# Optimization experiments

Measured on AMD Instinct MI355X. Metric: run time of the kernel, lower is better.

The kernel has to match this reference:

```python
import jax, jax.numpy as jnp
import numpy as np

B, T, K = 32, 512, 48
START_TAG, STOP_TAG = 46, 47


def setup_inputs() -> dict:
    key = jax.random.key(0)
    k1, k2, k3 = jax.random.split(key, 3)
    features = jax.random.normal(k1, (B, T, K, K), dtype=jnp.float32)
    targets = jax.random.randint(k2, (B, T), 0, K * K)  # flattened (from,to) index
    # lengths in [1, T], sorted descending (pack_padded_sequence convention)
    lengths = jnp.sort(jax.random.randint(k3, (B,), 1, T + 1))[::-1]
    return {"features": features, "targets": targets, "lengths": lengths}


def reference(features, targets, lengths):
    b, t_max, k, _ = features.shape
    # gold score: gather flattened target index per (b, t), masked by length
    flat = features.reshape(b, t_max, k * k)
    scores_at_targets = jnp.take_along_axis(flat, targets[:, :, None], axis=2)[:, :, 0]
    valid = jnp.arange(t_max)[None, :] < lengths[:, None]  # [B, T]
    gold_score = jnp.sum(jnp.where(valid, scores_at_targets, jnp.zeros((), features.dtype)))

    # forward (log-partition) recurrence; t=0 initializes from START row (all lengths >= 1)
    init = features[:, 0, START_TAG, :]  # [B, K]

    def step(carry, inp):
        feat_t, t = inp  # feat_t: [B, K, K] (prev_tag, cur_tag)
        cand = jax.nn.logsumexp(feat_t + carry[:, :, None], axis=1)  # [B, K]
        carry = jnp.where((t < lengths)[:, None], cand, carry)
        return carry, None

    feats_rest = jnp.moveaxis(features[:, 1:], 1, 0)  # [T-1, B, K, K]
    ts = jnp.arange(1, t_max)
    final, _ = jax.lax.scan(step, init, (feats_rest, ts))

    all_paths_scores = jnp.sum(final[:, STOP_TAG])
    return (all_paths_scores - gold_score) / b
```

## Files before the change

### kernel.cpp

```cpp
#include <hip/hip_runtime.h>

#define BB 32
#define TT 512
#define KK 48
#define KK2 2304
#define START_TAG 46
#define STOP_TAG 47
#define L2E 1.4426950408889634f
#define LN2 0.6931471805599453f
#define SLAB 7

__device__ inline float fast_exp2(float x) {
#if __has_builtin(__builtin_amdgcn_exp2f)
  return __builtin_amdgcn_exp2f(x);
#else
  return exp2f(x);
#endif
}
__device__ inline float fast_log2(float x) {
#if __has_builtin(__builtin_amdgcn_logf)
  return __builtin_amdgcn_logf(x);
#else
  return log2f(x);
#endif
}

template <int CTRL>
__device__ inline float dppf(float v) {
  int i = __float_as_int(v);
  int r = __builtin_amdgcn_update_dpp(i, i, CTRL, 0xF, 0xF, false);
  return __int_as_float(r);
}

__global__ __launch_bounds__(192, 1) void crf_kernel(
    const float* __restrict__ feat,
    const int* __restrict__ targets,
    const int* __restrict__ lengths,
    float* __restrict__ ws,
    float* __restrict__ out) {

  __shared__ float fbuf[2][SLAB * KK2];
  __shared__ float carry_g[2][KK];
  __shared__ float red[4];

  const int b   = blockIdx.x;
  const int len = lengths[b];
  const int tid = threadIdx.x;
  const int w   = tid >> 6;
  const int l   = tid & 63;
  const int j0  = l >> 2;
  const int ig  = l & 3;
  const int j   = w * 16 + j0;
  const float* fb = feat + (size_t)b * TT * KK2;

  float gsum = 0.f;
  for (int t = tid; t < TT; t += 192)
    if (t < len) gsum += fb[(size_t)t * KK2 + targets[b * TT + t]];
  #pragma unroll
  for (int m = 1; m < 64; m <<= 1) gsum += __shfl_xor(gsum, m, 64);
  if (l == 0) red[w] = gsum;

  if (tid < KK)
    carry_g[0][(tid & 3) * 12 + (tid >> 2)] = fb[START_TAG * KK + tid] * L2E;

  const int nsteps = len - 1;
  const int nslab  = (nsteps + SLAB - 1) / SLAB;

  auto stage_slab = [&](int s, int buf) {
    #pragma unroll
    for (int u = 0; u < SLAB; ++u) {
      int t = s * SLAB + 1 + u;
      if (t > len - 1) t = len - 1;
      #pragma unroll
      for (int q = 0; q < 3; ++q) {
        const float* gq = fb + (size_t)t * KK2 + (q * 16 + j0) * KK + w * 16 + ig * 4;
        float* d = &fbuf[buf][u * KK2 + w * 768 + q * 256];
        __builtin_amdgcn_global_load_lds(
            (const __attribute__((address_space(1))) unsigned int*)(const void*)gq,
            (__attribute__((address_space(3))) unsigned int*)(void*)d,
            16, 0, 0);
      }
    }
  };

  if (nsteps > 0) stage_slab(0, 0);
  __syncthreads();
  const float gold_b = red[0] + red[1] + red[2];

  for (int s = 0; s < nslab; ++s) {
    const int buf = s & 1;
    if (s + 1 < nslab) stage_slab(s + 1, buf ^ 1);
    const int base = s * SLAB + 1;
    const float* fs = &fbuf[buf][w * 768];

    float x[2][12];
    #pragma unroll
    for (int r = 0; r < 12; ++r) x[0][r] = fs[(r * 4 + ig) * 16 + j0];

    #pragma unroll
    for (int u = 0; u < SLAB; ++u) {
      const int t = base + u;
      if (t < len) {
        const int rd = (t - 1) & 1, wr = t & 1;

        float c[12];
        #pragma unroll
        for (int q = 0; q < 3; ++q) {
          float4 cv = *reinterpret_cast<const float4*>(&carry_g[rd][ig * 12 + q * 4]);
          c[q * 4 + 0] = cv.x; c[q * 4 + 1] = cv.y;
          c[q * 4 + 2] = cv.z; c[q * 4 + 3] = cv.w;
        }

        float xv[12];
        #pragma unroll
        for (int r = 0; r < 12; ++r) xv[r] = fmaf(x[u & 1][r], L2E, c[r]);

        if (u + 1 < SLAB) {
          #pragma unroll
          for (int r = 0; r < 12; ++r)
            x[(u + 1) & 1][r] = fs[(u + 1) * KK2 + (r * 4 + ig) * 16 + j0];
        }

        float m0 = fmaxf(fmaxf(xv[0], xv[1]), fmaxf(xv[2], xv[3]));
        float m1 = fmaxf(fmaxf(xv[4], xv[5]), fmaxf(xv[6], xv[7]));
        float m2 = fmaxf(fmaxf(xv[8], xv[9]), fmaxf(xv[10], xv[11]));
        float m = fmaxf(fmaxf(m0, m1), m2);
        m = fmaxf(m, dppf<0xB1>(m));
        m = fmaxf(m, dppf<0x4E>(m));

        float s0 = 0.f, s1 = 0.f, s2 = 0.f, s3 = 0.f;
        #pragma unroll
        for (int r = 0; r < 12; r += 4) {
          s0 += fast_exp2(xv[r + 0] - m);
          s1 += fast_exp2(xv[r + 1] - m);
          s2 += fast_exp2(xv[r + 2] - m);
          s3 += fast_exp2(xv[r + 3] - m);
        }
        float sm = (s0 + s1) + (s2 + s3);
        sm += dppf<0xB1>(sm);
        sm += dppf<0x4E>(sm);
        float cn = m + fast_log2(sm);

        if (ig == 0) carry_g[wr][(j & 3) * 12 + (j >> 2)] = cn;

        if (u == SLAB - 1) {
          asm volatile("s_waitcnt vmcnt(0) lgkmcnt(0)" ::: "memory");
        } else {
          asm volatile("s_waitcnt lgkmcnt(0)" ::: "memory");
        }
        __builtin_amdgcn_s_barrier();
      }
    }
  }

  if (tid == 0) {
    const int rdf = (len - 1) & 1;
    float v = carry_g[rdf][47] * LN2 - gold_b;
    atomicAdd(&ws[0], v);
    __threadfence();
    int done = atomicAdd((int*)&ws[1], 1);
    if (done == BB - 1) out[0] = atomicAdd(&ws[0], 0.0f) / (float)BB;
  }
}

extern "C" void kernel_launch(void* const* d_in, const int* in_sizes, int n_in,
                              void* d_out, int out_size, void* d_ws, size_t ws_size,
                              hipStream_t stream) {
  const float* feat  = (const float*)d_in[0];
  const int* targets = (const int*)d_in[1];
  const int* lengths = (const int*)d_in[2];
  float* ws  = (float*)d_ws;
  float* out = (float*)d_out;

  hipMemsetAsync(d_ws, 0, 16, stream);
  crf_kernel<<<BB, 192, 0, stream>>>(feat, targets, lengths, ws, out);
}
```

Before: 395.1 us.

## Stream features into registers via buffer loads and use lagged logsumexp shift

Replaces the LDS slab staging with raw buffer_load_dword instructions that land feature values directly in registers. Four per-step register sets are kept in flight, and an explicit vmcnt wait gates their use. The logsumexp now subtracts a running per-column shift taken from the previous step's max, so the exp/sum work no longer waits on the current step's max reduction. This shortens the serial chain per timestep and frees LDS. The cost is higher register pressure, hand-tuned waitcnt counts and a possible loss of numerical range if the lagged shift drifts from the true max.

```diff
diff --git a/kernel.cpp b/kernel.cpp
--- a/kernel.cpp
+++ b/kernel.cpp
@@ -8,7 +8,8 @@
 #define STOP_TAG 47
 #define L2E 1.4426950408889634f
 #define LN2 0.6931471805599453f
-#define SLAB 7
+
+typedef int v4i __attribute__((ext_vector_type(4)));
 
 __device__ inline float fast_exp2(float x) {
 #if __has_builtin(__builtin_amdgcn_exp2f)
@@ -32,6 +33,59 @@
   return __int_as_float(r);
 }
 
+
+#define BL(dst, OFFLIT)                                                      \
+  asm volatile("buffer_load_dword %0, %1, %2, 0 offen offset:" OFFLIT        \
+               : "=v"(dst) : "v"(voff), "s"(rsrc))
+#define LOAD12(P) do {                                                       \
+  BL(P##0, "0");    BL(P##1, "192");  BL(P##2, "384");  BL(P##3, "576");     \
+  BL(P##4, "768");  BL(P##5, "960");  BL(P##6, "1152"); BL(P##7, "1344");    \
+  BL(P##8, "1536"); BL(P##9, "1728"); BL(P##10, "1920"); BL(P##11, "2112");  \
+  voff += (unsigned)(KK2 * 4);                                               \
+} while (0)
+
+#define STEP(P, TCUR) do {                                                   \
+  const int _rd = ((TCUR) - 1) & 1, _wr = (TCUR) & 1;                        \
+  float4 _c0 = *(const float4*)&carry_g[_rd][ig * 12 + 0];                   \
+  float4 _c1 = *(const float4*)&carry_g[_rd][ig * 12 + 4];                   \
+  float4 _c2 = *(const float4*)&carry_g[_rd][ig * 12 + 8];                   \
+  asm volatile("s_waitcnt vmcnt(36)" ::: "memory");                          \
+  __builtin_amdgcn_sched_barrier(0);                                         \
+  float _f0 = fmaf(P##0, L2E, -shift),  _f1 = fmaf(P##1, L2E, -shift);       \
+  float _f2 = fmaf(P##2, L2E, -shift),  _f3 = fmaf(P##3, L2E, -shift);       \
+  float _f4 = fmaf(P##4, L2E, -shift),  _f5 = fmaf(P##5, L2E, -shift);       \
+  float _f6 = fmaf(P##6, L2E, -shift),  _f7 = fmaf(P##7, L2E, -shift);       \
+  float _f8 = fmaf(P##8, L2E, -shift),  _f9 = fmaf(P##9, L2E, -shift);       \
+  float _f10 = fmaf(P##10, L2E, -shift), _f11 = fmaf(P##11, L2E, -shift);    \
+  LOAD12(P); \
+  float _y0 = _c0.x + _f0,  _y1 = _c0.y + _f1;                               \
+  float _y2 = _c0.z + _f2,  _y3 = _c0.w + _f3;                               \
+  float _y4 = _c1.x + _f4,  _y5 = _c1.y + _f5;                               \
+  float _y6 = _c1.z + _f6,  _y7 = _c1.w + _f7;                               \
+  float _y8 = _c2.x + _f8,  _y9 = _c2.y + _f9;                               \
+  float _y10 = _c2.z + _f10, _y11 = _c2.w + _f11;                            \
+  float _eA = (fast_exp2(_y0) + fast_exp2(_y1)) +                            \
+              (fast_exp2(_y2) + fast_exp2(_y3));                             \
+  float _eB = (fast_exp2(_y4) + fast_exp2(_y5)) +                            \
+              (fast_exp2(_y6) + fast_exp2(_y7));                             \
+  float _eC = (fast_exp2(_y8) + fast_exp2(_y9)) +                            \
+              (fast_exp2(_y10) + fast_exp2(_y11));                           \
+  float _ss = _eA + _eB + _eC;                                               \
+  _ss += dppf<0xB1>(_ss);                                                    \
+  _ss += dppf<0x4E>(_ss);                                                    \
+  float _mA = fmaxf(fmaxf(_y0, _y1), fmaxf(_y2, _y3));                       \
+  float _mB = fmaxf(fmaxf(_y4, _y5), fmaxf(_y6, _y7));                       \
+  float _mC = fmaxf(fmaxf(_y8, _y9), fmaxf(_y10, _y11));                     \
+  float _mm = fmaxf(fmaxf(_mA, _mB), _mC);                                   \
+  _mm = fmaxf(_mm, dppf<0xB1>(_mm));                                         \
+  _mm = fmaxf(_mm, dppf<0x4E>(_mm));                                         \
+  float _cn = shift + fast_log2(_ss);                                        \
+  shift = shift + _mm;                 \
+  if (ig == 0) carry_g[_wr][j] = _cn;                                        \
+  asm volatile("s_waitcnt lgkmcnt(0)" ::: "memory");                         \
+  __builtin_amdgcn_s_barrier();                                              \
+} while (0)
+
 __global__ __launch_bounds__(192, 1) void crf_kernel(
     const float* __restrict__ feat,
     const int* __restrict__ targets,
@@ -39,7 +93,6 @@
     float* __restrict__ ws,
     float* __restrict__ out) {
 
-  __shared__ float fbuf[2][SLAB * KK2];
   __shared__ float carry_g[2][KK];
   __shared__ float red[4];
 
@@ -57,105 +110,42 @@
   for (int t = tid; t < TT; t += 192)
     if (t < len) gsum += fb[(size_t)t * KK2 + targets[b * TT + t]];
   #pragma unroll
-  for (int m = 1; m < 64; m <<= 1) gsum += __shfl_xor(gsum, m, 64);
+  for (int mk = 1; mk < 64; mk <<= 1) gsum += __shfl_xor(gsum, mk, 64);
   if (l == 0) red[w] = gsum;
 
-  if (tid < KK)
-    carry_g[0][(tid & 3) * 12 + (tid >> 2)] = fb[START_TAG * KK + tid] * L2E;
+  if (tid < KK) carry_g[0][tid] = fb[START_TAG * KK + tid] * L2E;
+  float shift = fb[START_TAG * KK + j] * L2E;
 
-  const int nsteps = len - 1;
-  const int nslab  = (nsteps + SLAB - 1) / SLAB;
-
-  auto stage_slab = [&](int s, int buf) {
-    #pragma unroll
-    for (int u = 0; u < SLAB; ++u) {
-      int t = s * SLAB + 1 + u;
-      if (t > len - 1) t = len - 1;
-      #pragma unroll
-      for (int q = 0; q < 3; ++q) {
-        const float* gq = fb + (size_t)t * KK2 + (q * 16 + j0) * KK + w * 16 + ig * 4;
-        float* d = &fbuf[buf][u * KK2 + w * 768 + q * 256];
-        __builtin_amdgcn_global_load_lds(
-            (const __attribute__((address_space(1))) unsigned int*)(const void*)gq,
-            (__attribute__((address_space(3))) unsigned int*)(void*)d,
-            16, 0, 0);
-      }
-    }
-  };
-
-  if (nsteps > 0) stage_slab(0, 0);
   __syncthreads();
   const float gold_b = red[0] + red[1] + red[2];
 
-  for (int s = 0; s < nslab; ++s) {
-    const int buf = s & 1;
-    if (s + 1 < nslab) stage_slab(s + 1, buf ^ 1);
-    const int base = s * SLAB + 1;
-    const float* fs = &fbuf[buf][w * 768];
+  union { const float* p; unsigned int u[2]; } ba; ba.p = fb;
+  v4i rsrc;
+  rsrc.x = (int)ba.u[0];
+  rsrc.y = (int)(ba.u[1] & 0xFFFFu);
+  rsrc.z = (int)((unsigned)(BB - b) * TT * KK2 * 4);
+  rsrc.w = 0x00020000;
 
-    float x[2][12];
-    #pragma unroll
-    for (int r = 0; r < 12; ++r) x[0][r] = fs[(r * 4 + ig) * 16 + j0];
+  unsigned int voff = (unsigned)(KK2 * 4) + (unsigned)(ig * 12 * KK * 4)
+                    + (unsigned)(j * 4);
 
-    #pragma unroll
-    for (int u = 0; u < SLAB; ++u) {
-      const int t = base + u;
-      if (t < len) {
-        const int rd = (t - 1) & 1, wr = t & 1;
+  float pa0,pa1,pa2,pa3,pa4,pa5,pa6,pa7,pa8,pa9,pa10,pa11;
+  float pb0,pb1,pb2,pb3,pb4,pb5,pb6,pb7,pb8,pb9,pb10,pb11;
+  float pc0,pc1,pc2,pc3,pc4,pc5,pc6,pc7,pc8,pc9,pc10,pc11;
+  float pd0,pd1,pd2,pd3,pd4,pd5,pd6,pd7,pd8,pd9,pd10,pd11;
+  LOAD12(pa); LOAD12(pb); LOAD12(pc); LOAD12(pd);
 
-        float c[12];
-        #pragma unroll
-        for (int q = 0; q < 3; ++q) {
-          float4 cv = *reinterpret_cast<const float4*>(&carry_g[rd][ig * 12 + q * 4]);
-          c[q * 4 + 0] = cv.x; c[q * 4 + 1] = cv.y;
-          c[q * 4 + 2] = cv.z; c[q * 4 + 3] = cv.w;
-        }
-
-        float xv[12];
-        #pragma unroll
-        for (int r = 0; r < 12; ++r) xv[r] = fmaf(x[u & 1][r], L2E, c[r]);
-
-        if (u + 1 < SLAB) {
-          #pragma unroll
-          for (int r = 0; r < 12; ++r)
-            x[(u + 1) & 1][r] = fs[(u + 1) * KK2 + (r * 4 + ig) * 16 + j0];
-        }
-
-        float m0 = fmaxf(fmaxf(xv[0], xv[1]), fmaxf(xv[2], xv[3]));
-        float m1 = fmaxf(fmaxf(xv[4], xv[5]), fmaxf(xv[6], xv[7]));
-        float m2 = fmaxf(fmaxf(xv[8], xv[9]), fmaxf(xv[10], xv[11]));
-        float m = fmaxf(fmaxf(m0, m1), m2);
-        m = fmaxf(m, dppf<0xB1>(m));
-        m = fmaxf(m, dppf<0x4E>(m));
-
-        float s0 = 0.f, s1 = 0.f, s2 = 0.f, s3 = 0.f;
-        #pragma unroll
-        for (int r = 0; r < 12; r += 4) {
-          s0 += fast_exp2(xv[r + 0] - m);
-          s1 += fast_exp2(xv[r + 1] - m);
-          s2 += fast_exp2(xv[r + 2] - m);
-          s3 += fast_exp2(xv[r + 3] - m);
-        }
-        float sm = (s0 + s1) + (s2 + s3);
-        sm += dppf<0xB1>(sm);
-        sm += dppf<0x4E>(sm);
-        float cn = m + fast_log2(sm);
-
-        if (ig == 0) carry_g[wr][(j & 3) * 12 + (j >> 2)] = cn;
-
-        if (u == SLAB - 1) {
-          asm volatile("s_waitcnt vmcnt(0) lgkmcnt(0)" ::: "memory");
-        } else {
-          asm volatile("s_waitcnt lgkmcnt(0)" ::: "memory");
-        }
-        __builtin_amdgcn_s_barrier();
-      }
-    }
+  for (int tb = 1; tb < len; tb += 4) {
+    { STEP(pa, tb); }
+    if (tb + 1 < len) { STEP(pb, tb + 1); }
+    if (tb + 2 < len) { STEP(pc, tb + 2); }
+    if (tb + 3 < len) { STEP(pd, tb + 3); }
   }
+  asm volatile("s_waitcnt vmcnt(0)" ::: "memory");
 
   if (tid == 0) {
     const int rdf = (len - 1) & 1;
-    float v = carry_g[rdf][47] * LN2 - gold_b;
+    float v = carry_g[rdf][STOP_TAG] * LN2 - gold_b;
     atomicAdd(&ws[0], v);
     __threadfence();
     int done = atomicAdd((int*)&ws[1], 1);
```

Measured after the change: 389.7 us. No clear change (-1.4%).
